# Performance work log

Hardware: AMD Instinct MI355X
Metric: run time of the kernel (lower is better)

Reference implementation:

```python
import jax, jax.numpy as jnp
import numpy as np

LOOKAHEAD = 12
H1 = 8          # f1_num_neurons
H2 = 8          # f2_num_neurons
N, S = 4_000_000, 16


def _linear_init(k, out_f, in_f):
    # matches torch nn.Linear default init: U(-1/sqrt(in), 1/sqrt(in))
    bound = 1.0 / np.sqrt(in_f)
    kw, kb = jax.random.split(k)
    W = jax.random.uniform(kw, (out_f, in_f), jnp.float32, -bound, bound)
    b = jax.random.uniform(kb, (out_f,), jnp.float32, -bound, bound)
    return W, b


def setup_inputs() -> dict:
    key = jax.random.key(0)
    ks = jax.random.split(key, 8)
    # monotone positive event times so log(diff + 0.1) is finite
    gaps = jax.random.uniform(ks[0], (N, S), jnp.float32, 0.05, 1.0)
    Y_seq = jnp.cumsum(gaps, axis=1)
    tau_vec = jax.random.uniform(ks[1], (N, 1), jnp.float32, 0.01, 1.0)
    f1_W, f1_b = _linear_init(ks[2], H1, H1 + 1)
    f2tau_W, f2tau_b = _linear_init(ks[3], H2, 1)
    f2_0_W, f2_0_b = _linear_init(ks[4], H2, H1)
    f2_1_W, f2_1_b = _linear_init(ks[5], H2, H2)
    f2_2_W, f2_2_b = _linear_init(ks[6], 1, H2)
    return dict(Y_seq=Y_seq, tau_vec=tau_vec,
                f1_W=f1_W, f1_b=f1_b,
                f2tau_W=f2tau_W, f2tau_b=f2tau_b,
                f2_0_W=f2_0_W, f2_0_b=f2_0_b,
                f2_1_W=f2_1_W, f2_1_b=f2_1_b,
                f2_2_W=f2_2_W, f2_2_b=f2_2_b)


def reference(Y_seq, tau_vec, f1_W, f1_b, f2tau_W, f2tau_b,
              f2_0_W, f2_0_b, f2_1_W, f2_1_b, f2_2_W, f2_2_b):
    n = Y_seq.shape[0]
    # log inter-event gaps over the last lookahead window: [n, LOOKAHEAD]
    Y_diff = jnp.log(jnp.diff(Y_seq[:, -LOOKAHEAD - 1:], axis=1) + 0.1)

    # f1: recurrent concat + shared Linear(H1+1 -> H1) + tanh, lookahead-1 steps
    def step(flow, y_col):                      # flow [n,H1], y_col [n]
        inp = jnp.concatenate([flow, y_col[:, None]], axis=1)  # [n, H1+1]
        return jnp.tanh(inp @ f1_W.T + f1_b), None

    flow0 = jnp.zeros((n, H1), Y_seq.dtype)
    flow, _ = jax.lax.scan(step, flow0, Y_diff[:, :LOOKAHEAD - 1].T)

    sp = jax.nn.softplus  # = log(1 + exp(x))
    # f2 layer 0: unconstrained weights plus softplus-constrained tau branch
    flow = flow @ f2_0_W.T + f2_0_b + tau_vec @ sp(f2tau_W).T + sp(f2tau_b)
    flow = jnp.tanh(flow)
    # hidden layer with softplus-reparameterized (positive) weights
    flow = jnp.tanh(flow @ sp(f2_1_W).T + sp(f2_1_b))
    # output layer, positive weights, softplus output activation
    flow = flow @ sp(f2_2_W).T + sp(f2_2_b)
    return sp(flow)  # [n, 1] cumulative hazard
```

## Files before the change

kernel.cpp:

```cpp
#include <hip/hip_runtime.h>
#include <stdint.h>

#define LOG2E 1.4426950408889634f
#define LN2   0.6931471805599453f

__device__ __forceinline__ float fast_tanh(float x) {
    float e = __builtin_amdgcn_exp2f(x * (2.0f * LOG2E));
    return 1.0f - 2.0f * __builtin_amdgcn_rcpf(e + 1.0f);
}
__device__ __forceinline__ float fast_softplus(float x) {
    float ax = fabsf(x);
    float t = LN2 * __builtin_amdgcn_logf(1.0f + __builtin_amdgcn_exp2f(-LOG2E * ax));
    return fmaxf(x, 0.0f) + t;
}
__device__ __forceinline__ float fast_ln(float x) {
    return LN2 * __builtin_amdgcn_logf(x);
}

__device__ __forceinline__ float uload(const float* __restrict__ p) {
    return __int_as_float(__builtin_amdgcn_readfirstlane(__float_as_int(*p)));
}

__global__ void prep_kernel(
    const float* __restrict__ f1W,  const float* __restrict__ f1b,
    const float* __restrict__ f2tW, const float* __restrict__ f2tb,
    const float* __restrict__ f20W, const float* __restrict__ f20b,
    const float* __restrict__ f21W, const float* __restrict__ f21b,
    const float* __restrict__ f22W, const float* __restrict__ f22b,
    float* __restrict__ w)
{
    int t = threadIdx.x;
    if (t < 72) w[t]        = f1W[t];
    if (t < 8)  w[72 + t]   = f1b[t];
    if (t < 64) w[80 + t]   = f20W[t];
    if (t < 8)  w[144 + t]  = f20b[t];
    if (t < 8)  w[152 + t]  = fast_softplus(f2tW[t]);
    if (t < 8)  w[160 + t]  = fast_softplus(f2tb[t]);
    if (t < 64) w[168 + t]  = fast_softplus(f21W[t]);
    if (t < 8)  w[232 + t]  = fast_softplus(f21b[t]);
    if (t < 8)  w[240 + t]  = fast_softplus(f22W[t]);
    if (t == 0) w[248]      = fast_softplus(f22b[0]);
}

__global__ void __launch_bounds__(256) haz_kernel(
    const float* __restrict__ Y,
    const float* __restrict__ tau,
    const float* __restrict__ w,
    float* __restrict__ out,
    int n)
{
    int i = blockIdx.x * blockDim.x + threadIdx.x;
    if (i >= n) return;

    union { float4 v[4]; float s[16]; } u;
    const float4* yp = (const float4*)(Y + (size_t)i * 16);
    u.v[0] = yp[0];
    u.v[1] = yp[1];
    u.v[2] = yp[2];
    u.v[3] = yp[3];

    float yd[11];
    #pragma unroll
    for (int j = 0; j < 11; ++j)
        yd[j] = fast_ln(u.s[4 + j] - u.s[3 + j] + 0.1f);

    float f1W[72], f1b[8];
    #pragma unroll
    for (int k = 0; k < 72; ++k) f1W[k] = uload(w + k);
    #pragma unroll
    for (int k = 0; k < 8; ++k)  f1b[k] = uload(w + 72 + k);

    float flow[8];
    #pragma unroll
    for (int k = 0; k < 8; ++k) flow[k] = 0.0f;

    #pragma unroll
    for (int t = 0; t < 11; ++t) {
        float nf[8];
        #pragma unroll
        for (int o = 0; o < 8; ++o) {
            float acc = f1b[o];
            #pragma unroll
            for (int k = 0; k < 8; ++k) acc = fmaf(f1W[o * 9 + k], flow[k], acc);
            acc = fmaf(f1W[o * 9 + 8], yd[t], acc);
            nf[o] = fast_tanh(acc);
        }
        #pragma unroll
        for (int o = 0; o < 8; ++o) flow[o] = nf[o];
    }

    float tv = tau[i];
    float h[8];
    #pragma unroll
    for (int o = 0; o < 8; ++o) {
        float acc = uload(w + 144 + o) + tv * uload(w + 152 + o) + uload(w + 160 + o);
        #pragma unroll
        for (int k = 0; k < 8; ++k) acc = fmaf(uload(w + 80 + o * 8 + k), flow[k], acc);
        h[o] = fast_tanh(acc);
    }
    float g[8];
    #pragma unroll
    for (int o = 0; o < 8; ++o) {
        float acc = uload(w + 232 + o);
        #pragma unroll
        for (int k = 0; k < 8; ++k) acc = fmaf(uload(w + 168 + o * 8 + k), h[k], acc);
        g[o] = fast_tanh(acc);
    }
    float z = uload(w + 248);
    #pragma unroll
    for (int k = 0; k < 8; ++k) z = fmaf(uload(w + 240 + k), g[k], z);

    out[i] = fast_softplus(z);
}

extern "C" void kernel_launch(void* const* d_in, const int* in_sizes, int n_in,
                              void* d_out, int out_size, void* d_ws, size_t ws_size,
                              hipStream_t stream)
{
    const float* Y   = (const float*)d_in[0];
    const float* tau = (const float*)d_in[1];
    float* w = (float*)d_ws;
    float* out = (float*)d_out;
    int n = in_sizes[1];

    prep_kernel<<<1, 128, 0, stream>>>(
        (const float*)d_in[2],  (const float*)d_in[3],
        (const float*)d_in[4],  (const float*)d_in[5],
        (const float*)d_in[6],  (const float*)d_in[7],
        (const float*)d_in[8],  (const float*)d_in[9],
        (const float*)d_in[10], (const float*)d_in[11],
        w);

    haz_kernel<<<(n + 255) / 256, 256, 0, stream>>>(Y, tau, w, out, n);
}
```

Measured before the change: 462.2 us.

## Process two rows per thread with packed FP32 math and polynomial tanh

Each thread now handles two rows, holding their state in 2-wide float vectors so the matrix-vector FMAs can map to packed FP32 instructions (v_pk_fma_f32). The exp/rcp-based tanh is replaced by a clamped Padé rational approximation whose reciprocal comes from a bit-trick seed refined by two Newton steps, so all of it runs on packed FMAs and none on the transcendental unit. This targets ALU and transcendental throughput in the recurrent loop. The cost is higher register pressure, half as many threads, and tanh accuracy that depends on the Padé approximant and its clamp.

Measured after the change: 469.6 us. About the same (+1.6%).

```diff
diff --git a/kernel.cpp b/kernel.cpp
--- a/kernel.cpp
+++ b/kernel.cpp
@@ -4,10 +4,6 @@
 #define LOG2E 1.4426950408889634f
 #define LN2   0.6931471805599453f
 
-__device__ __forceinline__ float fast_tanh(float x) {
-    float e = __builtin_amdgcn_exp2f(x * (2.0f * LOG2E));
-    return 1.0f - 2.0f * __builtin_amdgcn_rcpf(e + 1.0f);
-}
 __device__ __forceinline__ float fast_softplus(float x) {
     float ax = fabsf(x);
     float t = LN2 * __builtin_amdgcn_logf(1.0f + __builtin_amdgcn_exp2f(-LOG2E * ax));
@@ -19,6 +15,38 @@
 
 __device__ __forceinline__ float uload(const float* __restrict__ p) {
     return __int_as_float(__builtin_amdgcn_readfirstlane(__float_as_int(*p)));
+}
+
+typedef float        v2f __attribute__((ext_vector_type(2)));
+typedef unsigned int v2u __attribute__((ext_vector_type(2)));
+
+__device__ __forceinline__ v2f splat(float s) { return (v2f){s, s}; }
+__device__ __forceinline__ v2f vfma(v2f a, v2f b, v2f c) {
+    return __builtin_elementwise_fma(a, b, c);
+}
+
+__device__ __forceinline__ v2f pk_rcp(v2f d) {
+    union { v2f f; v2u u; } a;
+    a.f = d;
+    a.u = (v2u){0x7EF311C3u, 0x7EF311C3u} - a.u;
+    v2f x = a.f;
+    v2f e = vfma(-d, x, splat(1.0f));
+    x = vfma(x, e, x);
+    e = vfma(-d, x, splat(1.0f));
+    x = vfma(x, e, x);
+    return x;
+}
+
+__device__ __forceinline__ v2f pk_tanh(v2f x) {
+    x = __builtin_elementwise_min(__builtin_elementwise_max(x, splat(-4.7f)), splat(4.7f));
+    v2f t = x * x;
+    v2f num = vfma(t, splat(21.0f), splat(1260.0f));
+    num = vfma(t, num, splat(10395.0f));
+    num = num * x;
+    v2f den = t + splat(210.0f);
+    den = vfma(t, den, splat(4725.0f));
+    den = vfma(t, den, splat(10395.0f));
+    return num * pk_rcp(den);
 }
 
 __global__ void prep_kernel(
@@ -47,22 +75,27 @@
     const float* __restrict__ tau,
     const float* __restrict__ w,
     float* __restrict__ out,
-    int n)
+    int npairs, int n)
 {
     int i = blockIdx.x * blockDim.x + threadIdx.x;
-    if (i >= n) return;
+    if (i >= npairs) return;
+    int r0 = 2 * i;
+    bool has1 = (r0 + 1) < n;
+    int r1 = has1 ? r0 + 1 : r0;
 
-    union { float4 v[4]; float s[16]; } u;
-    const float4* yp = (const float4*)(Y + (size_t)i * 16);
-    u.v[0] = yp[0];
-    u.v[1] = yp[1];
-    u.v[2] = yp[2];
-    u.v[3] = yp[3];
+    union R { float4 v[4]; float s[16]; };
+    R A, B;
+    const float4* ya = (const float4*)(Y + (size_t)r0 * 16);
+    const float4* yb = (const float4*)(Y + (size_t)r1 * 16);
+    A.v[0] = ya[0]; A.v[1] = ya[1]; A.v[2] = ya[2]; A.v[3] = ya[3];
+    B.v[0] = yb[0]; B.v[1] = yb[1]; B.v[2] = yb[2]; B.v[3] = yb[3];
 
-    float yd[11];
+    v2f yd[11];
     #pragma unroll
-    for (int j = 0; j < 11; ++j)
-        yd[j] = fast_ln(u.s[4 + j] - u.s[3 + j] + 0.1f);
+    for (int j = 0; j < 11; ++j) {
+        yd[j] = (v2f){ fast_ln(A.s[4 + j] - A.s[3 + j] + 0.1f),
+                       fast_ln(B.s[4 + j] - B.s[3 + j] + 0.1f) };
+    }
 
     float f1W[72], f1b[8];
     #pragma unroll
@@ -70,47 +103,58 @@
     #pragma unroll
     for (int k = 0; k < 8; ++k)  f1b[k] = uload(w + 72 + k);
 
-    float flow[8];
+    v2f flow[8];
     #pragma unroll
-    for (int k = 0; k < 8; ++k) flow[k] = 0.0f;
+    for (int k = 0; k < 8; ++k) flow[k] = splat(0.0f);
 
     #pragma unroll
     for (int t = 0; t < 11; ++t) {
-        float nf[8];
+        v2f nf[8];
         #pragma unroll
         for (int o = 0; o < 8; ++o) {
-            float acc = f1b[o];
+            v2f acc = splat(f1b[o]);
             #pragma unroll
-            for (int k = 0; k < 8; ++k) acc = fmaf(f1W[o * 9 + k], flow[k], acc);
-            acc = fmaf(f1W[o * 9 + 8], yd[t], acc);
-            nf[o] = fast_tanh(acc);
+            for (int k = 0; k < 8; ++k)
+                acc = vfma(splat(f1W[o * 9 + k]), flow[k], acc);
+            acc = vfma(splat(f1W[o * 9 + 8]), yd[t], acc);
+            nf[o] = pk_tanh(acc);
         }
         #pragma unroll
         for (int o = 0; o < 8; ++o) flow[o] = nf[o];
     }
 
-    float tv = tau[i];
-    float h[8];
+    v2f tv = (v2f){ tau[r0], tau[r1] };
+    v2f h[8];
     #pragma unroll
     for (int o = 0; o < 8; ++o) {
-        float acc = uload(w + 144 + o) + tv * uload(w + 152 + o) + uload(w + 160 + o);
+        v2f acc = vfma(tv, splat(uload(w + 152 + o)),
+                       splat(uload(w + 144 + o) + uload(w + 160 + o)));
         #pragma unroll
-        for (int k = 0; k < 8; ++k) acc = fmaf(uload(w + 80 + o * 8 + k), flow[k], acc);
-        h[o] = fast_tanh(acc);
+        for (int k = 0; k < 8; ++k)
+            acc = vfma(splat(uload(w + 80 + o * 8 + k)), flow[k], acc);
+        h[o] = pk_tanh(acc);
     }
-    float g[8];
+    v2f g[8];
     #pragma unroll
     for (int o = 0; o < 8; ++o) {
-        float acc = uload(w + 232 + o);
+        v2f acc = splat(uload(w + 232 + o));
         #pragma unroll
-        for (int k = 0; k < 8; ++k) acc = fmaf(uload(w + 168 + o * 8 + k), h[k], acc);
-        g[o] = fast_tanh(acc);
+        for (int k = 0; k < 8; ++k)
+            acc = vfma(splat(uload(w + 168 + o * 8 + k)), h[k], acc);
+        g[o] = pk_tanh(acc);
     }
-    float z = uload(w + 248);
+    v2f z = splat(uload(w + 248));
     #pragma unroll
-    for (int k = 0; k < 8; ++k) z = fmaf(uload(w + 240 + k), g[k], z);
+    for (int k = 0; k < 8; ++k)
+        z = vfma(splat(uload(w + 240 + k)), g[k], z);
 
-    out[i] = fast_softplus(z);
+    float o0 = fast_softplus(z.x);
+    float o1 = fast_softplus(z.y);
+    if (has1) {
+        ((float2*)out)[i] = make_float2(o0, o1);
+    } else {
+        out[r0] = o0;
+    }
 }
 
 extern "C" void kernel_launch(void* const* d_in, const int* in_sizes, int n_in,
@@ -122,6 +166,7 @@
     float* w = (float*)d_ws;
     float* out = (float*)d_out;
     int n = in_sizes[1];
+    int npairs = (n + 1) / 2;
 
     prep_kernel<<<1, 128, 0, stream>>>(
         (const float*)d_in[2],  (const float*)d_in[3],
@@ -131,5 +176,5 @@
         (const float*)d_in[10], (const float*)d_in[11],
         w);
 
-    haz_kernel<<<(n + 255) / 256, 256, 0, stream>>>(Y, tau, w, out, n);
+    haz_kernel<<<(npairs + 255) / 256, 256, 0, stream>>>(Y, tau, w, out, npairs, n);
 }
```

## Run f1 recurrence in packed fp16 over row pairs with Pade tanh

Applied to the files above, without the earlier changes.

Each thread now handles two rows and packs them into half2 lanes, so the 11-step f1 recurrence runs on packed fp16 FMAs and a packed Pade tanh approximation that uses a bit-trick reciprocal refined by Newton steps. The prep kernel stores f1 weights as duplicated fp16 pairs. The f2 head stays in fp32 but also switches to a Pade tanh instead of the exp2/rcp form. This halves the VALU instruction count of the recurrence and removes transcendental calls, at the cost of fp16 accuracy in the recurrence, half as many threads, and larger per-thread loads.

After: 464.1 us. No clear change (+0.4%).

```diff
diff --git a/kernel.cpp b/kernel.cpp
--- a/kernel.cpp
+++ b/kernel.cpp
@@ -4,10 +4,6 @@
 #define LOG2E 1.4426950408889634f
 #define LN2   0.6931471805599453f
 
-__device__ __forceinline__ float fast_tanh(float x) {
-    float e = __builtin_amdgcn_exp2f(x * (2.0f * LOG2E));
-    return 1.0f - 2.0f * __builtin_amdgcn_rcpf(e + 1.0f);
-}
 __device__ __forceinline__ float fast_softplus(float x) {
     float ax = fabsf(x);
     float t = LN2 * __builtin_amdgcn_logf(1.0f + __builtin_amdgcn_exp2f(-LOG2E * ax));
@@ -19,6 +15,50 @@
 
 __device__ __forceinline__ float uload(const float* __restrict__ p) {
     return __int_as_float(__builtin_amdgcn_readfirstlane(__float_as_int(*p)));
+}
+
+__device__ __forceinline__ float tanh_pade(float x) {
+    x = fminf(fmaxf(x, -4.7f), 4.7f);
+    float t = x * x;
+    float num = fmaf(t, 21.0f, 1260.0f);
+    num = fmaf(t, num, 10395.0f);
+    num *= x;
+    float den = t + 210.0f;
+    den = fmaf(t, den, 4725.0f);
+    den = fmaf(t, den, 10395.0f);
+    float r = __int_as_float(0x7EF311C3u - __float_as_uint(den));
+    r = fmaf(r, fmaf(-den, r, 1.0f), r);
+    r = fmaf(r, fmaf(-den, r, 1.0f), r);
+    return num * r;
+}
+
+typedef _Float16 v2h __attribute__((ext_vector_type(2)));
+
+__device__ __forceinline__ v2h hfma(v2h a, v2h b, v2h c) {
+    return __builtin_elementwise_fma(a, b, c);
+}
+__device__ __forceinline__ v2h hsplat(float s) {
+    _Float16 h = (_Float16)s;
+    return (v2h){h, h};
+}
+
+__device__ __forceinline__ v2h pk_tanh(v2h x) {
+    const v2h ONE = hsplat(1.0f);
+    x = __builtin_elementwise_min(__builtin_elementwise_max(x, hsplat(-4.7f)), hsplat(4.7f));
+    v2h t = x * x;
+    v2h num = hfma(t, hsplat(0.00202020f), hsplat(0.12121212f));
+    num = hfma(t, num, ONE);
+    num = num * x;
+    v2h den = hfma(t, hsplat(9.62001e-5f), hsplat(0.02020202f));
+    den = hfma(t, den, hsplat(0.45454545f));
+    den = hfma(t, den, ONE);
+    union { v2h h; unsigned int u; } a;
+    a.h = den;
+    a.u = 0x77997799u - a.u;
+    v2h r = a.h;
+    r = hfma(r, hfma(-den, r, ONE), r);
+    r = hfma(r, hfma(-den, r, ONE), r);
+    return num * r;
 }
 
 __global__ void prep_kernel(
@@ -30,8 +70,9 @@
     float* __restrict__ w)
 {
     int t = threadIdx.x;
-    if (t < 72) w[t]        = f1W[t];
-    if (t < 8)  w[72 + t]   = f1b[t];
+    union { v2h h; float f; } p;
+    if (t < 72) { _Float16 h = (_Float16)f1W[t]; p.h = (v2h){h, h}; w[t] = p.f; }
+    if (t < 8)  { _Float16 h = (_Float16)f1b[t]; p.h = (v2h){h, h}; w[72 + t] = p.f; }
     if (t < 64) w[80 + t]   = f20W[t];
     if (t < 8)  w[144 + t]  = f20b[t];
     if (t < 8)  w[152 + t]  = fast_softplus(f2tW[t]);
@@ -42,75 +83,99 @@
     if (t == 0) w[248]      = fast_softplus(f22b[0]);
 }
 
+__device__ __forceinline__ float f2_head(const float* __restrict__ w,
+                                         const float fl[8], float tv) {
+    float h[8];
+    #pragma unroll
+    for (int o = 0; o < 8; ++o) {
+        float acc = uload(w + 144 + o) + tv * uload(w + 152 + o) + uload(w + 160 + o);
+        #pragma unroll
+        for (int k = 0; k < 8; ++k) acc = fmaf(uload(w + 80 + o * 8 + k), fl[k], acc);
+        h[o] = tanh_pade(acc);
+    }
+    float g[8];
+    #pragma unroll
+    for (int o = 0; o < 8; ++o) {
+        float acc = uload(w + 232 + o);
+        #pragma unroll
+        for (int k = 0; k < 8; ++k) acc = fmaf(uload(w + 168 + o * 8 + k), h[k], acc);
+        g[o] = tanh_pade(acc);
+    }
+    float z = uload(w + 248);
+    #pragma unroll
+    for (int k = 0; k < 8; ++k) z = fmaf(uload(w + 240 + k), g[k], z);
+    return fast_softplus(z);
+}
+
 __global__ void __launch_bounds__(256) haz_kernel(
     const float* __restrict__ Y,
     const float* __restrict__ tau,
     const float* __restrict__ w,
     float* __restrict__ out,
-    int n)
+    int npairs, int n)
 {
     int i = blockIdx.x * blockDim.x + threadIdx.x;
-    if (i >= n) return;
-
-    union { float4 v[4]; float s[16]; } u;
-    const float4* yp = (const float4*)(Y + (size_t)i * 16);
-    u.v[0] = yp[0];
-    u.v[1] = yp[1];
-    u.v[2] = yp[2];
-    u.v[3] = yp[3];
-
-    float yd[11];
-    #pragma unroll
-    for (int j = 0; j < 11; ++j)
-        yd[j] = fast_ln(u.s[4 + j] - u.s[3 + j] + 0.1f);
-
-    float f1W[72], f1b[8];
-    #pragma unroll
-    for (int k = 0; k < 72; ++k) f1W[k] = uload(w + k);
-    #pragma unroll
-    for (int k = 0; k < 8; ++k)  f1b[k] = uload(w + 72 + k);
-
-    float flow[8];
-    #pragma unroll
-    for (int k = 0; k < 8; ++k) flow[k] = 0.0f;
+    if (i >= npairs) return;
+    int r0 = 2 * i;
+    bool has1 = (r0 + 1) < n;
+    int r1 = has1 ? r0 + 1 : r0;
+
+    union R { float4 v[4]; float s[16]; };
+    R A, B;
+    const float4* ya = (const float4*)(Y + (size_t)r0 * 16);
+    const float4* yb = (const float4*)(Y + (size_t)r1 * 16);
+    A.v[0] = ya[0]; A.v[1] = ya[1]; A.v[2] = ya[2]; A.v[3] = ya[3];
+    B.v[0] = yb[0]; B.v[1] = yb[1]; B.v[2] = yb[2]; B.v[3] = yb[3];
+
+    v2h yd[11];
+    #pragma unroll
+    for (int j = 0; j < 11; ++j) {
+        float da = fast_ln(A.s[4 + j] - A.s[3 + j] + 0.1f);
+        float db = fast_ln(B.s[4 + j] - B.s[3 + j] + 0.1f);
+        yd[j] = (v2h){(_Float16)da, (_Float16)db};
+    }
+
+    v2h Wk[72], Bk[8];
+    #pragma unroll
+    for (int k = 0; k < 72; ++k) {
+        union { float f; v2h h; } c; c.f = uload(w + k); Wk[k] = c.h;
+    }
+    #pragma unroll
+    for (int k = 0; k < 8; ++k) {
+        union { float f; v2h h; } c; c.f = uload(w + 72 + k); Bk[k] = c.h;
+    }
+
+    v2h flow[8];
+    #pragma unroll
+    for (int k = 0; k < 8; ++k) flow[k] = hsplat(0.0f);
 
     #pragma unroll
     for (int t = 0; t < 11; ++t) {
-        float nf[8];
+        v2h nf[8];
         #pragma unroll
         for (int o = 0; o < 8; ++o) {
-            float acc = f1b[o];
+            v2h acc = Bk[o];
             #pragma unroll
-            for (int k = 0; k < 8; ++k) acc = fmaf(f1W[o * 9 + k], flow[k], acc);
-            acc = fmaf(f1W[o * 9 + 8], yd[t], acc);
-            nf[o] = fast_tanh(acc);
+            for (int k = 0; k < 8; ++k) acc = hfma(Wk[o * 9 + k], flow[k], acc);
+            acc = hfma(Wk[o * 9 + 8], yd[t], acc);
+            nf[o] = pk_tanh(acc);
         }
         #pragma unroll
         for (int o = 0; o < 8; ++o) flow[o] = nf[o];
     }
 
-    float tv = tau[i];
-    float h[8];
-    #pragma unroll
-    for (int o = 0; o < 8; ++o) {
-        float acc = uload(w + 144 + o) + tv * uload(w + 152 + o) + uload(w + 160 + o);
-        #pragma unroll
-        for (int k = 0; k < 8; ++k) acc = fmaf(uload(w + 80 + o * 8 + k), flow[k], acc);
-        h[o] = fast_tanh(acc);
-    }
-    float g[8];
-    #pragma unroll
-    for (int o = 0; o < 8; ++o) {
-        float acc = uload(w + 232 + o);
-        #pragma unroll
-        for (int k = 0; k < 8; ++k) acc = fmaf(uload(w + 168 + o * 8 + k), h[k], acc);
-        g[o] = fast_tanh(acc);
-    }
-    float z = uload(w + 248);
-    #pragma unroll
-    for (int k = 0; k < 8; ++k) z = fmaf(uload(w + 240 + k), g[k], z);
-
-    out[i] = fast_softplus(z);
+    float flA[8], flB[8];
+    #pragma unroll
+    for (int k = 0; k < 8; ++k) { flA[k] = (float)flow[k].x; flB[k] = (float)flow[k].y; }
+
+    float o0 = f2_head(w, flA, tau[r0]);
+    float o1 = f2_head(w, flB, tau[r1]);
+
+    if (has1) {
+        ((float2*)out)[i] = make_float2(o0, o1);
+    } else {
+        out[r0] = o0;
+    }
 }
 
 extern "C" void kernel_launch(void* const* d_in, const int* in_sizes, int n_in,
@@ -122,6 +187,7 @@
     float* w = (float*)d_ws;
     float* out = (float*)d_out;
     int n = in_sizes[1];
+    int npairs = (n + 1) / 2;
 
     prep_kernel<<<1, 128, 0, stream>>>(
         (const float*)d_in[2],  (const float*)d_in[3],
@@ -131,5 +197,5 @@
         (const float*)d_in[10], (const float*)d_in[11],
         w);
 
-    haz_kernel<<<(n + 255) / 256, 256, 0, stream>>>(Y, tau, w, out, n);
-}
+    haz_kernel<<<(npairs + 255) / 256, 256, 0, stream>>>(Y, tau, w, out, npairs, n);
+}
```
